# Kernel optimization log

Hardware: AMD Instinct MI355X
Metric: run time of the kernel (lower is better)

## Reference

```python
import jax, jax.numpy as jnp
import numpy as np
from jax import lax

B = 2; H = 96; W = 96
WS = 8; SHIFT = WS // 2; NW = H // WS; P = WS * WS
NH = 3; HD = 32; CD = 96; TD = 96
MID = 2 * CD; GA = 16; BASES = 16

def _rel_index():
    g = np.stack(np.meshgrid(np.arange(WS), np.arange(WS), indexing='ij'), -1).reshape(-1, 2)
    rel = g[:, None, :] - g[None, :, :] + WS - 1
    return jnp.asarray(rel[..., 0] * (2 * WS - 1) + rel[..., 1])  # [P, P]

REL_IDX = _rel_index()

def _sw_mask():
    m = np.zeros((NW, NW, WS, WS, WS, WS), bool); s = WS - SHIFT
    m[-1, :, :s, :, s:, :] = True
    m[-1, :, s:, :, :s, :] = True
    m[:, -1, :, :s, :, s:] = True
    m[:, -1, :, s:, :, :s] = True
    return jnp.asarray(m.reshape(NW * NW, P, P))

SW_MASK = _sw_mask()

def _ln(x, g, b, eps=1e-5):
    mu = x.mean(-1, keepdims=True)
    v = ((x - mu) ** 2).mean(-1, keepdims=True)
    return (x - mu) * lax.rsqrt(v + eps) * g + b

def _conv1x1(x, w):
    return jnp.einsum('bchw,oc->bohw', x, w)

def _conv3x3(x, w, b=None, groups=1):
    y = lax.conv_general_dilated(x, w, (1, 1), ((1, 1), (1, 1)),
                                 dimension_numbers=('NCHW', 'OIHW', 'NCHW'),
                                 feature_group_count=groups)
    return y if b is None else y + b[None, :, None, None]

def _unfold3(x):
    # torch F.unfold(k=3,p=1): channel-major patch order (c, kh, kw)
    bs, c, h, w = x.shape
    xp = jnp.pad(x, ((0, 0), (0, 0), (1, 1), (1, 1)))
    pats = jnp.stack([xp[:, :, i:i + h, j:j + w] for i in range(3) for j in range(3)], axis=2)
    return pats.reshape(bs, c * 9, h * w)

def _adaconv(x, ada_w, p1w, p1b, p2w, p2b):
    bs, c, h, w = x.shape
    para = jax.nn.relu(_conv1x1(x, p1w) + p1b[None, :, None, None])
    para = _conv3x3(para, p2w, p2b).reshape(bs, BASES, h * w)      # [b, r, p]
    xu = _unfold3(x).reshape(bs, GA, (c // GA) * 9, h * w)          # [b, g, d, p]
    # out[b,g,o,p] = sum_{d,r} ada_w[g,o,d,r] * xu[b,g,d,p] * para[b,r,p]
    t = jnp.einsum('godr,bgdp->bgorp', ada_w, xu)
    out = jnp.einsum('bgorp,brp->bgop', t, para)
    return out.reshape(bs, c, h, w)

def _conv_block(x, ln_g, ln_b, c1_pw, c1_dw, c2_pw, ada_w, p1w, p1b, p2w, p2b, c3_w):
    r = _ln(x.transpose(0, 2, 3, 1), ln_g, ln_b).transpose(0, 3, 1, 2)
    b1 = _conv3x3(_conv1x1(r, c1_pw), c1_dw, groups=MID)
    b2 = jax.nn.gelu(_adaconv(_conv1x1(r, c2_pw), ada_w, p1w, p1b, p2w, p2b), approximate=False)
    return x + _conv1x1(b1 * b2, c3_w)

def _wmsa(x, qkv_w, qkv_b, rel_pos, proj_w, proj_b):
    bs = x.shape[0]
    x = jnp.roll(x, (-SHIFT, -SHIFT), (1, 2))
    qkv = jnp.einsum('bhwc,oc->bhwo', x, qkv_w) + qkv_b
    qkv = qkv.reshape(bs, NW, WS, NW, WS, 3, NH, HD)
    qkv = qkv.transpose(5, 6, 0, 1, 3, 2, 4, 7).reshape(3, NH, bs, NW * NW, P, HD)
    q, k, v = qkv[0], qkv[1], qkv[2]
    sim = jnp.einsum('hbwpc,hbwqc->hbwpq', q, k) * (HD ** -0.5)
    bias = rel_pos[REL_IDX.reshape(-1)].reshape(P, P, NH).transpose(2, 0, 1)
    sim = sim + bias[:, None, None]
    sim = jnp.where(SW_MASK[None, None], -jnp.inf, sim)
    attn = jax.nn.softmax(sim, axis=-1)
    out = jnp.einsum('hbwpq,hbwqc->hbwpc', attn, v)
    out = out.reshape(NH, bs, NW, NW, WS, WS, HD).transpose(1, 2, 4, 3, 5, 0, 6).reshape(bs, H, W, NH * HD)
    out = jnp.einsum('bhwc,oc->bhwo', out, proj_w) + proj_b
    return jnp.roll(out, (SHIFT, SHIFT), (1, 2))

def _swin_block(x, ln1_g, ln1_b, qkv_w, qkv_b, rel_pos, proj_w, proj_b,
                ln2_g, ln2_b, f_w1, f_b1, f_dw, f_db, f_w2, f_b2):
    xt = x.transpose(0, 2, 3, 1)  # b h w c
    xt = xt + _wmsa(_ln(xt, ln1_g, ln1_b), qkv_w, qkv_b, rel_pos, proj_w, proj_b)
    y = _ln(xt, ln2_g, ln2_b).transpose(0, 3, 1, 2)
    y = _conv1x1(y, f_w1) + f_b1[None, :, None, None]
    y = _conv3x3(y, f_dw, f_db, groups=2 * TD)
    y = jax.nn.gelu(y, approximate=False)
    y = _conv1x1(y, f_w2) + f_b2[None, :, None, None]
    xt = xt + y.transpose(0, 2, 3, 1)
    return xt.transpose(0, 3, 1, 2)

def _block(x, cb_ln_g, cb_ln_b, cb_c1_pw, cb_c1_dw, cb_c2_pw, ada_w, ada_p1_w, ada_p1_b,
           ada_p2_w, ada_p2_b, cb_c3_w, ln1_g, ln1_b, qkv_w, qkv_b, rel_pos, proj_w, proj_b,
           ln2_g, ln2_b, ffn_w1, ffn_b1, ffn_dw, ffn_db, ffn_w2, ffn_b2, out_w, out_b):
    conv_x, trans_x = x[:, :CD], x[:, CD:]
    conv_x = _conv_block(conv_x, cb_ln_g, cb_ln_b, cb_c1_pw, cb_c1_dw, cb_c2_pw,
                         ada_w, ada_p1_w, ada_p1_b, ada_p2_w, ada_p2_b, cb_c3_w)
    trans_x = _swin_block(trans_x, ln1_g, ln1_b, qkv_w, qkv_b, rel_pos, proj_w, proj_b,
                          ln2_g, ln2_b, ffn_w1, ffn_b1, ffn_dw, ffn_db, ffn_w2, ffn_b2)
    res = _conv1x1(jnp.concatenate([conv_x, trans_x], axis=1), out_w) + out_b[None, :, None, None]
    return x + res

def setup_inputs():
    key = jax.random.key(0)
    ks = jax.random.split(key, 20)
    n = lambda i, shape, s=0.05: jax.random.normal(ks[i], shape, jnp.float32) * s
    return {
        'x': jax.random.normal(ks[0], (B, CD + TD, H, W), jnp.float32),
        'cb_ln_g': jnp.ones((CD,), jnp.float32), 'cb_ln_b': jnp.zeros((CD,), jnp.float32),
        'cb_c1_pw': n(1, (MID, CD)), 'cb_c1_dw': n(2, (MID, 1, 3, 3)),
        'cb_c2_pw': n(3, (MID, CD)),
        'ada_w': n(4, (GA, MID // GA, (MID // GA) * 9, BASES)),
        'ada_p1_w': n(5, (BASES, MID)), 'ada_p1_b': jnp.zeros((BASES,), jnp.float32),
        'ada_p2_w': n(6, (BASES, BASES, 3, 3)), 'ada_p2_b': jnp.zeros((BASES,), jnp.float32),
        'cb_c3_w': n(7, (CD, MID)),
        'ln1_g': jnp.ones((TD,), jnp.float32), 'ln1_b': jnp.zeros((TD,), jnp.float32),
        'qkv_w': n(8, (3 * TD, TD)), 'qkv_b': jnp.zeros((3 * TD,), jnp.float32),
        'rel_pos': n(9, ((2 * WS - 1) ** 2, NH), 0.02),
        'proj_w': n(10, (TD, TD)), 'proj_b': jnp.zeros((TD,), jnp.float32),
        'ln2_g': jnp.ones((TD,), jnp.float32), 'ln2_b': jnp.zeros((TD,), jnp.float32),
        'ffn_w1': n(11, (2 * TD, TD)), 'ffn_b1': jnp.zeros((2 * TD,), jnp.float32),
        'ffn_dw': n(12, (2 * TD, 1, 3, 3)), 'ffn_db': jnp.zeros((2 * TD,), jnp.float32),
        'ffn_w2': n(13, (TD, 2 * TD)), 'ffn_b2': jnp.zeros((TD,), jnp.float32),
        'out_w': n(14, (CD + TD, CD + TD)), 'out_b': jnp.zeros((CD + TD,), jnp.float32),
    }

def reference(x, cb_ln_g, cb_ln_b, cb_c1_pw, cb_c1_dw, cb_c2_pw, ada_w, ada_p1_w, ada_p1_b,
              ada_p2_w, ada_p2_b, cb_c3_w, ln1_g, ln1_b, qkv_w, qkv_b, rel_pos, proj_w, proj_b,
              ln2_g, ln2_b, ffn_w1, ffn_b1, ffn_dw, ffn_db, ffn_w2, ffn_b2, out_w, out_b):
    return _block(x, cb_ln_g, cb_ln_b, cb_c1_pw, cb_c1_dw, cb_c2_pw, ada_w, ada_p1_w, ada_p1_b,
                  ada_p2_w, ada_p2_b, cb_c3_w, ln1_g, ln1_b, qkv_w, qkv_b, rel_pos, proj_w, proj_b,
                  ln2_g, ln2_b, ffn_w1, ffn_b1, ffn_dw, ffn_db, ffn_w2, ffn_b2, out_w, out_b)
```

## Files before the change

kernel.cpp:

```cpp
#include <hip/hip_runtime.h>
#include <math.h>

#define HW_ 9216
#define IH 96
#define IW 96
#define NB 2
#define ST (NB*HW_)

typedef __attribute__((ext_vector_type(8))) short bf16x8;
typedef __attribute__((ext_vector_type(4))) float f32x4;
typedef unsigned short u16;

__device__ __forceinline__ float gelu_f(float v){
  return 0.5f*v*(1.0f+erff(v*0.70710678118654752440f));
}
__device__ __forceinline__ unsigned f2bf(float f){
  unsigned u = __float_as_uint(f);
  return (u + 0x7FFF + ((u>>16)&1)) >> 16;
}
__device__ __forceinline__ float bfl(unsigned u){ return __uint_as_float(u<<16); }
__device__ __forceinline__ float bfh(unsigned u){ return __uint_as_float(u & 0xffff0000u); }

__global__ __launch_bounds__(256) void ln12_k(const float* __restrict__ x,
    const float* __restrict__ g1, const float* __restrict__ b1,
    const float* __restrict__ g2, const float* __restrict__ b2,
    u16* __restrict__ lnc, u16* __restrict__ ln1o,
    float* __restrict__ xc, float* __restrict__ xt)
{
  __shared__ float t[192][33];
  const int p0 = blockIdx.x<<5;
  const int bb = p0/HW_, hw0 = p0 - bb*HW_;
  const int tid = threadIdx.x;
  const int px = tid & 31, cr = tid >> 5;
  const float* xb = x + (size_t)bb*192*HW_ + hw0;
  #pragma unroll
  for (int k=0;k<24;k++){
    int c = cr + k*8;
    t[c][px] = xb[(size_t)c*HW_ + px];
  }
  __syncthreads();
  const int lane = tid&63, wv = tid>>6;
  #pragma unroll 1
  for (int i=0;i<8;i++){
    const int lp = wv*8+i;
    const size_t p = p0 + lp;
    float a0 = t[lane][lp];
    float a1 = (lane<32)? t[64+lane][lp] : 0.f;
    float c0 = t[96+lane][lp];
    float c1 = (lane<32)? t[160+lane][lp] : 0.f;
    float s1=a0+a1, s2=c0+c1;
    #pragma unroll
    for (int o=32;o;o>>=1){ s1+=__shfl_xor(s1,o); s2+=__shfl_xor(s2,o); }
    const float mu1=s1*(1.f/96.f), mu2=s2*(1.f/96.f);
    const float d0=a0-mu1, d1=a1-mu1, e0=c0-mu2, e1=c1-mu2;
    float q1=d0*d0+((lane<32)?d1*d1:0.f), q2=e0*e0+((lane<32)?e1*e1:0.f);
    #pragma unroll
    for (int o=32;o;o>>=1){ q1+=__shfl_xor(q1,o); q2+=__shfl_xor(q2,o); }
    const float r1=rsqrtf(q1*(1.f/96.f)+1e-5f), r2=rsqrtf(q2*(1.f/96.f)+1e-5f);
    lnc [p*96+lane] = (u16)f2bf(d0*r1*g1[lane]+b1[lane]);
    ln1o[p*96+lane] = (u16)f2bf(e0*r2*g2[lane]+b2[lane]);
    xc  [p*96+lane] = a0;
    xt  [p*96+lane] = c0;
    if (lane<32){
      lnc [p*96+64+lane] = (u16)f2bf(d1*r1*g1[64+lane]+b1[64+lane]);
      ln1o[p*96+64+lane] = (u16)f2bf(e1*r2*g2[64+lane]+b2[64+lane]);
      xc  [p*96+64+lane] = a1;
      xt  [p*96+64+lane] = c1;
    }
  }
}

__global__ __launch_bounds__(256) void ln_k(const float* __restrict__ in, int istride,
                                            const float* __restrict__ gam, const float* __restrict__ bet,
                                            u16* __restrict__ out){
  int lane = threadIdx.x & 63;
  int wv   = threadIdx.x >> 6;
  int p    = (blockIdx.x << 2) + wv;
  const float* row = in + (size_t)p*istride;
  float v0 = row[lane];
  float v1 = (lane < 32) ? row[64+lane] : 0.0f;
  float s = v0 + v1;
  #pragma unroll
  for (int o=32;o;o>>=1) s += __shfl_xor(s,o);
  float mu = s * (1.0f/96.0f);
  float d0 = v0 - mu;
  float d1 = v1 - mu;
  float qv = d0*d0 + ((lane<32)? d1*d1 : 0.0f);
  #pragma unroll
  for (int o=32;o;o>>=1) qv += __shfl_xor(qv,o);
  float rstd = rsqrtf(qv*(1.0f/96.0f) + 1e-5f);
  u16* orow = out + (size_t)p*96;
  orow[lane] = (u16)f2bf(d0*rstd*gam[lane] + bet[lane]);
  if (lane < 32) orow[64+lane] = (u16)f2bf(d1*rstd*gam[64+lane] + bet[64+lane]);
}

template<int ACT, bool CONCAT, bool FINAL, bool HASB, bool HASR, bool OUTBF, bool SPLIT>
__global__ __launch_bounds__(256) void conv_mfma_k(
    const u16* __restrict__ in1, const float* __restrict__ in2f, int istride,
    const u16* __restrict__ wbf, const float* __restrict__ bias,
    const float* __restrict__ res, int rstride,
    void* __restrict__ out, int ostride, int Cin, int Cout,
    u16* __restrict__ out2)
{
  __shared__ __align__(16) unsigned char smem[39936];
  unsigned char* actl = smem;
  unsigned char* wl   = smem + 26624;
  const int tid=threadIdx.x, lane=tid&63, wv=tid>>6;
  const int lr=lane&15, g4=lane>>4, wm=wv>>1, wn=wv&1;
  const int p0=blockIdx.x<<7, co0=blockIdx.y<<6;

  f32x4 acc[2][4];
  #pragma unroll
  for (int m=0;m<2;m++)
    #pragma unroll
    for (int n=0;n<4;n++) acc[m][n]=(f32x4){0.f,0.f,0.f,0.f};

  for (int kc=0; kc<Cin; kc+=96){
    {
      const int row=tid>>1, half=tid&1;
      if (!CONCAT || kc==0){
        const u16* rp = in1 + (size_t)(p0+row)*istride + (CONCAT?0:kc) + half*48;
        #pragma unroll
        for (int s=0;s<6;s++)
          *(uint4*)(actl + row*208 + (half*6+s)*16) = *(const uint4*)(rp + s*8);
      } else {
        const float* rp = in2f + (size_t)(p0+row)*96 + half*48;
        #pragma unroll
        for (int s=0;s<6;s++){
          float4 a=*(const float4*)(rp+s*8), b=*(const float4*)(rp+s*8+4);
          uint4 pk;
          pk.x=f2bf(a.x)|(f2bf(a.y)<<16);
          pk.y=f2bf(a.z)|(f2bf(a.w)<<16);
          pk.z=f2bf(b.x)|(f2bf(b.y)<<16);
          pk.w=f2bf(b.z)|(f2bf(b.w)<<16);
          *(uint4*)(actl + row*208 + (half*6+s)*16) = pk;
        }
      }
    }
    {
      const int row=tid&63, grp=tid>>6;
      const int co=co0+row;
      const u16* wr = wbf + (size_t)co*Cin + kc;
      #pragma unroll
      for (int s=0;s<3;s++){
        int sl=grp*3+s;
        uint4 v={0,0,0,0};
        if (co<Cout) v=*(const uint4*)(wr + sl*8);
        *(uint4*)(wl + row*208 + sl*16)=v;
      }
    }
    __syncthreads();
    #pragma unroll
    for (int ks=0;ks<3;ks++){
      const int sl=ks*4+g4;
      bf16x8 afr[2], bfr[4];
      #pragma unroll
      for (int m=0;m<2;m++) afr[m]=*(const bf16x8*)(wl + ((wm*2+m)*16+lr)*208 + sl*16);
      #pragma unroll
      for (int n=0;n<4;n++) bfr[n]=*(const bf16x8*)(actl + (wn*64+n*16+lr)*208 + sl*16);
      #pragma unroll
      for (int m=0;m<2;m++)
        #pragma unroll
        for (int n=0;n<4;n++)
          acc[m][n]=__builtin_amdgcn_mfma_f32_16x16x32_bf16(afr[m], bfr[n], acc[m][n],0,0,0);
    }
    __syncthreads();
  }

  if (FINAL){
    float* outf = (float*)out;
    #pragma unroll
    for (int m=0;m<2;m++){
      const int cb=co0+(wm*2+m)*16+(g4<<2);
      float4 bv = make_float4(0.f,0.f,0.f,0.f);
      if (HASB) bv = *(const float4*)(bias+cb);
      #pragma unroll
      for (int n=0;n<4;n++){
        const int p=p0+wn*64+n*16+lr;
        const int bb=p/HW_, hw=p-bb*HW_;
        const float av[4]={acc[m][n].x,acc[m][n].y,acc[m][n].z,acc[m][n].w};
        const float bvv[4]={bv.x,bv.y,bv.z,bv.w};
        #pragma unroll
        for (int j=0;j<4;j++){
          size_t oi=((size_t)bb*192+cb+j)*HW_+hw;
          outf[oi]=av[j]+bvv[j]+res[oi];
        }
      }
    }
    return;
  }
  float* lt=(float*)smem;
  #pragma unroll
  for (int m=0;m<2;m++)
    #pragma unroll
    for (int n=0;n<4;n++){
      int px=wn*64+n*16+lr;
      int c=(wm*2+m)*16+(g4<<2);
      *(f32x4*)&lt[px*68+c]=acc[m][n];
    }
  __syncthreads();
  {
    const int pr=tid>>1, half=tid&1;
    const int p=p0+pr;
    #pragma unroll
    for (int s=0;s<8;s++){
      int cl=half*32+s*4;
      int co=co0+cl;
      if (co<Cout){
        float4 v=*(float4*)&lt[pr*68+cl];
        if (SPLIT){
          if (co>=384){
            const int c2 = co-384;
            const float4 bv=*(const float4*)(bias+c2);
            v.x=fmaxf(v.x+bv.x,0.f); v.y=fmaxf(v.y+bv.y,0.f);
            v.z=fmaxf(v.z+bv.z,0.f); v.w=fmaxf(v.w+bv.w,0.f);
            uint2 pk;
            pk.x = f2bf(v.x)|(f2bf(v.y)<<16);
            pk.y = f2bf(v.z)|(f2bf(v.w)<<16);
            *(uint2*)((u16*)out + (size_t)p*16 + c2) = pk;
          } else {
            const int cc = (co<192)? co : co-192;
            const int gg = cc/12, cll = cc - gg*12;
            u16* dst = out2 + ((co<192)? (size_t)0 : (size_t)ST*192)
                     + ((size_t)gg*ST + p)*12 + cll;
            uint2 pk;
            pk.x = f2bf(v.x)|(f2bf(v.y)<<16);
            pk.y = f2bf(v.z)|(f2bf(v.w)<<16);
            *(uint2*)dst = pk;
          }
          continue;
        }
        if (HASB){ const float4 bv=*(const float4*)(bias+co); v.x+=bv.x;v.y+=bv.y;v.z+=bv.z;v.w+=bv.w; }
        if (ACT==1){
          v.x=fmaxf(v.x,0.f); v.y=fmaxf(v.y,0.f); v.z=fmaxf(v.z,0.f); v.w=fmaxf(v.w,0.f);
        }
        if (HASR){ const float4 rv=*(const float4*)(res+(size_t)p*rstride+co); v.x+=rv.x;v.y+=rv.y;v.z+=rv.z;v.w+=rv.w; }
        if (OUTBF){
          uint2 pk;
          pk.x = f2bf(v.x)|(f2bf(v.y)<<16);
          pk.y = f2bf(v.z)|(f2bf(v.w)<<16);
          *(uint2*)((u16*)out + (size_t)p*ostride + co) = pk;
        } else {
          *(float4*)((float*)out + (size_t)p*ostride + co) = v;
        }
      }
    }
  }
}

template<bool HASB, bool DOGELU>
__global__ __launch_bounds__(256) void dw3x3_k(const u16* __restrict__ in, int istride,
                                               const float* __restrict__ w,
                                               const float* __restrict__ bias,
                                               u16* __restrict__ out, int C){
  int t = blockIdx.x*256 + threadIdx.x;
  int cg = C >> 2;
  int p = t / cg;
  if (p >= ST) return;
  int c4 = (t - p*cg) << 2;
  int bb = p / HW_, hw = p - bb*HW_;
  int hy = hw / IW, wx = hw - hy*IW;
  float w0[9], w1[9], w2[9], w3[9];
  #pragma unroll
  for (int tp=0;tp<9;tp++){
    w0[tp]=w[(c4+0)*9+tp]; w1[tp]=w[(c4+1)*9+tp]; w2[tp]=w[(c4+2)*9+tp]; w3[tp]=w[(c4+3)*9+tp];
  }
  float ax=0.f, ay=0.f, az=0.f, aw=0.f;
  #pragma unroll
  for (int i=0;i<3;i++){
    int y = hy+i-1;
    if ((unsigned)y >= IH) continue;
    #pragma unroll
    for (int j=0;j<3;j++){
      int x2 = wx+j-1;
      if ((unsigned)x2 >= IW) continue;
      const uint2 r = *(const uint2*)(in + ((size_t)bb*HW_ + y*IW + x2)*istride + c4);
      int tp=i*3+j;
      ax += bfl(r.x)*w0[tp]; ay += bfh(r.x)*w1[tp];
      az += bfl(r.y)*w2[tp]; aw += bfh(r.y)*w3[tp];
    }
  }
  if (HASB){ ax+=bias[c4]; ay+=bias[c4+1]; az+=bias[c4+2]; aw+=bias[c4+3]; }
  if (DOGELU){ ax=gelu_f(ax); ay=gelu_f(ay); az=gelu_f(az); aw=gelu_f(aw); }
  uint2 pk;
  pk.x = f2bf(ax)|(f2bf(ay)<<16);
  pk.y = f2bf(az)|(f2bf(aw)<<16);
  *(uint2*)(out + (size_t)p*C + c4) = pk;
}

__global__ __launch_bounds__(256) void p2conv_k(const u16* __restrict__ in, const float* __restrict__ w,
                                                const float* __restrict__ bias, float* __restrict__ out){
  __shared__ float ws[2304];
  int tid = threadIdx.x;
  for (int i=tid;i<2304;i+=256) ws[i]=w[i];
  __syncthreads();
  int gidx = blockIdx.x*256 + tid;
  int p = gidx >> 2, qq = gidx & 3;
  int bb = p / HW_, hw = p - bb*HW_;
  int hy = hw / IW, wx = hw - hy*IW;
  const int cb = qq<<2;
  float a0=bias[cb], a1=bias[cb+1], a2=bias[cb+2], a3=bias[cb+3];
  #pragma unroll
  for (int i=0;i<3;i++){
    int y=hy+i-1; if ((unsigned)y>=IH) continue;
    #pragma unroll
    for (int j=0;j<3;j++){
      int x2=wx+j-1; if ((unsigned)x2>=IW) continue;
      int tap=i*3+j;
      const uint4 r = *(const uint4*)(in + ((size_t)bb*HW_ + y*IW + x2)*16);
      const uint4 r2 = *(const uint4*)(in + ((size_t)bb*HW_ + y*IW + x2)*16 + 8);
      float vv[16]={bfl(r.x),bfh(r.x),bfl(r.y),bfh(r.y),bfl(r.z),bfh(r.z),bfl(r.w),bfh(r.w),
                    bfl(r2.x),bfh(r2.x),bfl(r2.y),bfh(r2.y),bfl(r2.z),bfh(r2.z),bfl(r2.w),bfh(r2.w)};
      #pragma unroll
      for (int ci=0;ci<16;ci++){
        float v = vv[ci];
        a0 += ws[(cb+0)*144 + ci*9 + tap]*v;
        a1 += ws[(cb+1)*144 + ci*9 + tap]*v;
        a2 += ws[(cb+2)*144 + ci*9 + tap]*v;
        a3 += ws[(cb+3)*144 + ci*9 + tap]*v;
      }
    }
  }
  *(float4*)(out + (size_t)p*16 + cb) = make_float4(a0,a1,a2,a3);
}

__global__ __launch_bounds__(256) void allprep_k(
    const float* __restrict__ s0, const float* __restrict__ s1,
    const float* __restrict__ s2, const float* __restrict__ s3,
    const float* __restrict__ s4, const float* __restrict__ s5,
    const float* __restrict__ s6, const float* __restrict__ s7,
    const float* __restrict__ p1w, const float* __restrict__ aw,
    u16* __restrict__ wdst, u16* __restrict__ apre)
{
  const int bid = blockIdx.x, tid = threadIdx.x;
  if (bid < 648){
    const int blks[8]={108,72,72,72,36,72,72,144};
    const int off[8] ={0,27648,46080,66048,84480,93696,112128,130560};
    const int sz[8]  ={27648,18432,18432,18432,9216,18432,18432,36864};
    int m=0, acc=0;
    #pragma unroll
    for (int k=0;k<8;k++){ if (bid >= acc + blks[k]){ acc += blks[k]; m=k+1; } }
    const float* s = (m==0)?s0:(m==1)?s1:(m==2)?s2:(m==3)?s3:(m==4)?s4:(m==5)?s5:(m==6)?s6:s7;
    int i = (bid-acc)*256 + tid;
    if (i < sz[m]) wdst[off[m]+i] = (u16)f2bf(s[i]);
  } else if (bid < 654){
    int i = (bid-648)*256 + tid;
    if (i < 1536){
      int o = i/96, ci = i - o*96;
      float s = 0.f;
      for (int k=0;k<192;k++) s += p1w[o*192+k]*s2[k*96+ci];
      wdst[64512+i] = (u16)f2bf(s);
    }
  } else {
    int E = (bid-654)*256 + tid;
    int g = E / 30720, e = E - g*30720;
    int row = e / 160, kp = e - row*160;
    int tap = kp >> 4, cl = kp & 15;
    int o = row >> 4, r = row & 15;
    float v = 0.f;
    if (tap < 9 && cl < 12)
      v = aw[(((size_t)(g*12+o)*108) + cl*9 + tap)*16 + r];
    apre[(size_t)g*30720 + e] = (u16)f2bf(v);
  }
}

__global__ __launch_bounds__(256) void adaconv_mfma_k(
    const u16* __restrict__ x1g, const u16* __restrict__ x2g,
    const float* __restrict__ para, const u16* __restrict__ apre,
    const float* __restrict__ dww, u16* __restrict__ outb2)
{
  __shared__ __align__(16) unsigned char smem[34096];
  unsigned char* HB2 = smem;
  unsigned char* HB1 = smem + 8640;
  float* PS = (float*)(smem + 17280);
  float* OS = (float*)(smem + 27520);
  float* WDW = (float*)(smem + 33664);

  const int tid=threadIdx.x, lane=tid&63, wv=tid>>6;
  const int lr=lane&15, g4=lane>>4;
  const int hi=(lane>>5)&1, lo16=(lane>>4)&1;
  const int b=blockIdx.z, g=blockIdx.y, reg=blockIdx.x;
  const int rh=(reg/12)<<4, rw=(reg%12)<<3;

  bf16x8 af[3][5];
  {
    const u16* ag = apre + (size_t)g*30720;
    #pragma unroll
    for (int oo=0;oo<3;oo++){
      const int row=(wv*3+oo)*16+lr;
      #pragma unroll
      for (int ks=0;ks<5;ks++)
        af[oo][ks] = *(const bf16x8*)(ag + row*160 + ks*32 + g4*8);
    }
  }
  if (tid < 180){
    int hy = tid/10, hx = tid - hy*10;
    int gy = rh+hy-1, gx = rw+hx-1;
    uint2 a2={0,0},b2={0,0},c2={0,0}, a1={0,0},b1={0,0},c1={0,0};
    if ((unsigned)gy<IH && (unsigned)gx<IW){
      const size_t base = ((size_t)g*ST + (size_t)b*HW_ + gy*IW + gx)*12;
      const u16* s2 = x2g + base;
      a2=*(const uint2*)s2; b2=*(const uint2*)(s2+4); c2=*(const uint2*)(s2+8);
      const u16* s1 = x1g + base;
      a1=*(const uint2*)s1; b1=*(const uint2*)(s1+4); c1=*(const uint2*)(s1+8);
    }
    *(uint4*)(HB2 + tid*48)      = make_uint4(a2.x,a2.y,b2.x,b2.y);
    *(uint4*)(HB2 + tid*48 + 16) = make_uint4(c2.x,c2.y,0,0);
    *(uint4*)(HB1 + tid*48)      = make_uint4(a1.x,a1.y,b1.x,b1.y);
    *(uint4*)(HB1 + tid*48 + 16) = make_uint4(c1.x,c1.y,0,0);
  }
  if (tid < 108) WDW[tid] = dww[g*108 + tid];
  #pragma unroll
  for (int it=0; it<2; ++it){
    int idx = tid + (it<<8);
    int sub = idx >> 8;
    int p = (idx>>2)&63, q = idx&3;
    int gy = rh + (sub<<3) + (p>>3), gx = rw + (p&7);
    float4 v = *(const float4*)(para + ((size_t)b*HW_+gy*IW+gx)*16 + q*4);
    *(float4*)&PS[sub*1280 + p*20 + q*4] = v;
  }
  __syncthreads();

  int tapoff[5];
  tapoff[0] = hi ? 48   : 0;
  tapoff[1] = hi ? 480  : 96;
  tapoff[2] = hi ? 576  : 528;
  tapoff[3] = hi ? 1008 : 960;
  tapoff[4] = 1056;

  #pragma unroll
  for (int sub=0; sub<2; ++sub){
    const int sy = sub<<3;
    const int base0 = ((sy + (lr>>3))*10 + (lr&7))*48 + lo16*16;

    f32x4 acc[3][4];
    #pragma unroll
    for (int oo=0;oo<3;oo++)
      #pragma unroll
      for (int n=0;n<4;n++) acc[oo][n]=(f32x4){0.f,0.f,0.f,0.f};

    #pragma unroll
    for (int ks=0;ks<5;ks++){
      bf16x8 bfr[4];
      #pragma unroll
      for (int n=0;n<4;n++)
        bfr[n] = *(const bf16x8*)(HB2 + base0 + n*960 + tapoff[ks]);
      #pragma unroll
      for (int oo=0;oo<3;oo++)
        #pragma unroll
        for (int n=0;n<4;n++)
          acc[oo][n]=__builtin_amdgcn_mfma_f32_16x16x32_bf16(af[oo][ks], bfr[n], acc[oo][n],0,0,0);
    }

    const float* ps = &PS[sub*1280];
    #pragma unroll
    for (int oo=0;oo<3;oo++){
      const int o=wv*3+oo;
      #pragma unroll
      for (int n=0;n<4;n++){
        const int p=(n<<4)+lr;
        const f32x4 prv = *(const f32x4*)&ps[p*20+(g4<<2)];
        float s=acc[oo][n].x*prv.x+acc[oo][n].y*prv.y+acc[oo][n].z*prv.z+acc[oo][n].w*prv.w;
        s += __shfl_xor(s,16); s += __shfl_xor(s,32);
        if (g4==n) OS[((sub<<6)+p)*12+o] = gelu_f(s);
      }
    }
  }
  __syncthreads();
  {
    const size_t gb = (size_t)b*HW_;
    for (int idx=tid; idx<384; idx+=256){
      const int cq = idx % 3;
      const int rest = idx / 3;
      const int p = rest & 63, sub = rest >> 6;
      const int py = p>>3, px = p&7;
      const int Y = (sub<<3)+py, X = px;
      const unsigned char* hb1 = HB1 + (Y*10+X)*48 + cq*8;
      const float* wd = &WDW[cq*36];
      float v0=0.f,v1=0.f,v2=0.f,v3=0.f;
      #pragma unroll
      for (int i=0;i<3;i++){
        #pragma unroll
        for (int j=0;j<3;j++){
          const uint2 r = *(const uint2*)(hb1 + (i*10+j)*48);
          const int tp=i*3+j;
          v0 += bfl(r.x)*wd[tp];      v1 += bfh(r.x)*wd[9+tp];
          v2 += bfl(r.y)*wd[18+tp];   v3 += bfh(r.y)*wd[27+tp];
        }
      }
      const size_t gi = (gb + (rh+(sub<<3)+py)*IW + (rw+px))*192 + g*12 + cq*4;
      const float* os = &OS[((sub<<6)+p)*12 + cq*4];
      uint2 pk;
      pk.x = f2bf(os[0]*v0) | (f2bf(os[1]*v1)<<16);
      pk.y = f2bf(os[2]*v2) | (f2bf(os[3]*v3)<<16);
      *(uint2*)(outb2 + gi) = pk;
    }
  }
}

__global__ __launch_bounds__(64) void attn_k(const u16* __restrict__ qkv,
                                             const float* __restrict__ relpos,
                                             u16* __restrict__ outa){
  __shared__ float k_s[2048];
  __shared__ float v_s[2048];
  __shared__ float rel_s[225];
  const int win = blockIdx.x, head = blockIdx.y, b = blockIdx.z;
  const int wi = win/12, wj = win%12;
  const int lane = threadIdx.x;
  for (int i=lane;i<225;i+=64) rel_s[i] = relpos[i*3+head];
  const int pi = lane>>3, pj = lane&7;
  const int hr = wi*8+pi, wr = wj*8+pj;
  const int sh = (hr+4)%96, sw = (wr+4)%96;
  const size_t pix = (size_t)b*HW_ + sh*96 + sw;
  const u16* base = qkv + pix*288;
  const float SC = 0.17677669529663687f;
  float q[32];
  #pragma unroll
  for (int i=0;i<4;i++){
    const uint4 r = *(const uint4*)(base + head*32 + i*8);
    q[i*8+0]=bfl(r.x)*SC; q[i*8+1]=bfh(r.x)*SC;
    q[i*8+2]=bfl(r.y)*SC; q[i*8+3]=bfh(r.y)*SC;
    q[i*8+4]=bfl(r.z)*SC; q[i*8+5]=bfh(r.z)*SC;
    q[i*8+6]=bfl(r.w)*SC; q[i*8+7]=bfh(r.w)*SC;
  }
  #pragma unroll
  for (int i=0;i<4;i++){
    const uint4 rk = *(const uint4*)(base + 96 + head*32 + i*8);
    const uint4 rv = *(const uint4*)(base + 192 + head*32 + i*8);
    *(float4*)&k_s[(lane<<5)+i*8]   = make_float4(bfl(rk.x),bfh(rk.x),bfl(rk.y),bfh(rk.y));
    *(float4*)&k_s[(lane<<5)+i*8+4] = make_float4(bfl(rk.z),bfh(rk.z),bfl(rk.w),bfh(rk.w));
    *(float4*)&v_s[(lane<<5)+i*8]   = make_float4(bfl(rv.x),bfh(rv.x),bfl(rv.y),bfh(rv.y));
    *(float4*)&v_s[(lane<<5)+i*8+4] = make_float4(bfl(rv.z),bfh(rv.z),bfl(rv.w),bfh(rv.w));
  }
  __syncthreads();
  const bool mi = (wi==11), mj = (wj==11);
  float sc[64];
  #pragma unroll
  for (int qq=0; qq<64; qq++){
    const float4* kr4 = (const float4*)&k_s[qq<<5];
    float s = 0.f;
    #pragma unroll
    for (int i=0;i<8;i++){
      const float4 kv = kr4[i];
      s += q[4*i]*kv.x + q[4*i+1]*kv.y + q[4*i+2]*kv.z + q[4*i+3]*kv.w;
    }
    const int qi = qq>>3, qj = qq&7;
    s += rel_s[(pi-qi+7)*15 + (pj-qj+7)];
    const bool msk = (mi && ((pi<4)!=(qi<4))) || (mj && ((pj<4)!=(qj<4)));
    sc[qq] = msk ? -1e30f : s;
  }
  float m = sc[0];
  #pragma unroll
  for (int qq=1;qq<64;qq++) m = fmaxf(m, sc[qq]);
  float sum = 0.f;
  #pragma unroll
  for (int qq=0;qq<64;qq++){ float e = __expf(sc[qq]-m); sc[qq]=e; sum+=e; }
  const float inv = 1.f/sum;
  float acc[32];
  #pragma unroll
  for (int i=0;i<32;i++) acc[i]=0.f;
  #pragma unroll
  for (int qq=0;qq<64;qq++){
    const float a = sc[qq]*inv;
    const float4* vr4 = (const float4*)&v_s[qq<<5];
    #pragma unroll
    for (int i=0;i<8;i++){
      const float4 vv = vr4[i];
      acc[4*i]+=a*vv.x; acc[4*i+1]+=a*vv.y; acc[4*i+2]+=a*vv.z; acc[4*i+3]+=a*vv.w;
    }
  }
  u16* orow = outa + pix*96 + head*32;
  #pragma unroll
  for (int i=0;i<4;i++){
    uint4 pk;
    pk.x = f2bf(acc[i*8+0])|(f2bf(acc[i*8+1])<<16);
    pk.y = f2bf(acc[i*8+2])|(f2bf(acc[i*8+3])<<16);
    pk.z = f2bf(acc[i*8+4])|(f2bf(acc[i*8+5])<<16);
    pk.w = f2bf(acc[i*8+6])|(f2bf(acc[i*8+7])<<16);
    *(uint4*)(orow + i*8) = pk;
  }
}

extern "C" void kernel_launch(void* const* d_in, const int* in_sizes, int n_in,
                              void* d_out, int out_size, void* d_ws, size_t ws_size,
                              hipStream_t stream)
{
  (void)in_sizes; (void)n_in; (void)out_size; (void)ws_size;
  const float* x        = (const float*)d_in[0];
  const float* cb_ln_g  = (const float*)d_in[1];
  const float* cb_ln_b  = (const float*)d_in[2];
  const float* cb_c1_pw = (const float*)d_in[3];
  const float* cb_c1_dw = (const float*)d_in[4];
  const float* cb_c2_pw = (const float*)d_in[5];
  const float* ada_w    = (const float*)d_in[6];
  const float* ada_p1_w = (const float*)d_in[7];
  const float* ada_p1_b = (const float*)d_in[8];
  const float* ada_p2_w = (const float*)d_in[9];
  const float* ada_p2_b = (const float*)d_in[10];
  const float* cb_c3_w  = (const float*)d_in[11];
  const float* ln1_g    = (const float*)d_in[12];
  const float* ln1_b    = (const float*)d_in[13];
  const float* qkv_w    = (const float*)d_in[14];
  const float* qkv_b    = (const float*)d_in[15];
  const float* rel_pos  = (const float*)d_in[16];
  const float* proj_w   = (const float*)d_in[17];
  const float* proj_b   = (const float*)d_in[18];
  const float* ln2_g    = (const float*)d_in[19];
  const float* ln2_b    = (const float*)d_in[20];
  const float* ffn_w1   = (const float*)d_in[21];
  const float* ffn_b1   = (const float*)d_in[22];
  const float* ffn_dw   = (const float*)d_in[23];
  const float* ffn_db   = (const float*)d_in[24];
  const float* ffn_w2   = (const float*)d_in[25];
  const float* ffn_b2   = (const float*)d_in[26];
  const float* out_w    = (const float*)d_in[27];
  const float* out_b    = (const float*)d_in[28];

  char* wsb = (char*)d_ws;
  float* XC  = (float*)wsb;
  float* U0f = (float*)(wsb + (size_t)ST*96*4);
  float* XT  = (float*)(wsb + (size_t)ST*384*4);
  float* PA2 = (float*)(wsb + (size_t)ST*480*4);
  u16* B2b  = (u16*)(wsb + (size_t)ST*496*4);
  u16* LNCb = B2b  + (size_t)ST*192;
  u16* R4b  = LNCb + (size_t)ST*96;
  u16* R6b  = R4b  + (size_t)ST*96;
  u16* PA1b = R6b  + (size_t)ST*96;
  u16* Wbf  = PA1b + (size_t)ST*16;
  u16* Apre = Wbf + 167424;
  u16* X1G  = (u16*)U0f;
  u16* X2G  = X1G + (size_t)ST*192;
  u16* QKVb = (u16*)U0f;
  u16* FF1b = (u16*)U0f;
  u16* DWOb = (u16*)U0f + (size_t)ST*192;

  const u16* W_qkv  = Wbf + 0;
  const u16* W_c12p = Wbf + 27648;
  const u16* W_c3   = Wbf + 66048;
  const u16* W_proj = Wbf + 84480;
  const u16* W_ffn1 = Wbf + 93696;
  const u16* W_ffn2 = Wbf + 112128;
  const u16* W_fin  = Wbf + 130560;

  allprep_k<<<2574, 256, 0, stream>>>(qkv_w, cb_c1_pw, cb_c2_pw, cb_c3_w,
                                      proj_w, ffn_w1, ffn_w2, out_w,
                                      ada_p1_w, ada_w, Wbf, Apre);

  ln12_k<<<ST/32, 256, 0, stream>>>(x, cb_ln_g, cb_ln_b, ln1_g, ln1_b, LNCb, R6b, XC, XT);

  conv_mfma_k<0,false,false,false,false,true,true><<<dim3(ST/128, 7), 256, 0, stream>>>(LNCb, nullptr, 96, W_c12p, ada_p1_b, nullptr, 0, PA1b, 16, 96, 400, X1G);
  p2conv_k<<<(ST*4)/256, 256, 0, stream>>>(PA1b, ada_p2_w, ada_p2_b, PA2);
  adaconv_mfma_k<<<dim3(72, 16, NB), 256, 0, stream>>>(X1G, X2G, PA2, Apre, cb_c1_dw, B2b);
  conv_mfma_k<0,false,false,false,true,true,false><<<dim3(ST/128, 2), 256, 0, stream>>>(B2b, nullptr, 192, W_c3, nullptr, XC, 96, R4b, 96, 192, 96, nullptr);

  conv_mfma_k<0,false,false,true,false,true,false><<<dim3(ST/128, 5), 256, 0, stream>>>(R6b, nullptr, 96, W_qkv, qkv_b, nullptr, 0, QKVb, 288, 96, 288, nullptr);
  attn_k<<<dim3(144, 3, NB), 64, 0, stream>>>(QKVb, rel_pos, R6b);
  conv_mfma_k<0,false,false,true,true,false,false><<<dim3(ST/128, 2), 256, 0, stream>>>(R6b, nullptr, 96, W_proj, proj_b, XT, 96, XT, 96, 96, 96, nullptr);
  ln_k<<<ST/4, 256, 0, stream>>>(XT, 96, ln2_g, ln2_b, R6b);
  conv_mfma_k<0,false,false,true,false,true,false><<<dim3(ST/128, 3), 256, 0, stream>>>(R6b, nullptr, 96, W_ffn1, ffn_b1, nullptr, 0, FF1b, 192, 96, 192, nullptr);
  dw3x3_k<true,true><<<(ST*48)/256, 256, 0, stream>>>(FF1b, 192, ffn_dw, ffn_db, DWOb, 192);
  conv_mfma_k<0,false,false,true,true,false,false><<<dim3(ST/128, 2), 256, 0, stream>>>(DWOb, nullptr, 192, W_ffn2, ffn_b2, XT, 96, XT, 96, 192, 96, nullptr);

  conv_mfma_k<0,true,true,true,true,false,false><<<dim3(ST/128, 3), 256, 0, stream>>>(R4b, XT, 96, W_fin, out_b, x, 0, (float*)d_out, 0, 192, 192, nullptr);
}
```

Measured before the change: 230.1 us.

## Merge independent kernels into combined launches to cut launch count

Kernel bodies become device functions, and independent stages share one launch through block-index dispatch. Weight prep runs with the first LayerNorm, the adaconv-p1 GEMM with the QKV GEMM, adaconv with the attention projection, and conv3 with the second LayerNorm. Attention moves earlier, and QKV gets its own workspace region because it is now live at the same time as X1G. The aim is to remove launch gaps and let small grids fill the GPU together. The cost is a larger workspace footprint and mixed block types within one launch, which may share resources unevenly.

```diff
diff --git a/kernel.cpp b/kernel.cpp
--- a/kernel.cpp
+++ b/kernel.cpp
@@ -21,14 +21,14 @@
 __device__ __forceinline__ float bfl(unsigned u){ return __uint_as_float(u<<16); }
 __device__ __forceinline__ float bfh(unsigned u){ return __uint_as_float(u & 0xffff0000u); }
 
-__global__ __launch_bounds__(256) void ln12_k(const float* __restrict__ x,
+__device__ __forceinline__ void ln12_body(const float* __restrict__ x,
     const float* __restrict__ g1, const float* __restrict__ b1,
     const float* __restrict__ g2, const float* __restrict__ b2,
     u16* __restrict__ lnc, u16* __restrict__ ln1o,
-    float* __restrict__ xc, float* __restrict__ xt)
+    float* __restrict__ xc, float* __restrict__ xt, int bidx)
 {
   __shared__ float t[192][33];
-  const int p0 = blockIdx.x<<5;
+  const int p0 = bidx<<5;
   const int bb = p0/HW_, hw0 = p0 - bb*HW_;
   const int tid = threadIdx.x;
   const int px = tid & 31, cr = tid >> 5;
@@ -70,12 +70,13 @@
   }
 }
 
-__global__ __launch_bounds__(256) void ln_k(const float* __restrict__ in, int istride,
-                                            const float* __restrict__ gam, const float* __restrict__ bet,
-                                            u16* __restrict__ out){
+__device__ __forceinline__ void ln_body(const float* __restrict__ in, int istride,
+    const float* __restrict__ gam, const float* __restrict__ bet,
+    u16* __restrict__ out, int bidx)
+{
   int lane = threadIdx.x & 63;
   int wv   = threadIdx.x >> 6;
-  int p    = (blockIdx.x << 2) + wv;
+  int p    = (bidx << 2) + wv;
   const float* row = in + (size_t)p*istride;
   float v0 = row[lane];
   float v1 = (lane < 32) ? row[64+lane] : 0.0f;
@@ -95,19 +96,18 @@
 }
 
 template<int ACT, bool CONCAT, bool FINAL, bool HASB, bool HASR, bool OUTBF, bool SPLIT>
-__global__ __launch_bounds__(256) void conv_mfma_k(
+__device__ __forceinline__ void conv_body(unsigned char* smem,
     const u16* __restrict__ in1, const float* __restrict__ in2f, int istride,
     const u16* __restrict__ wbf, const float* __restrict__ bias,
     const float* __restrict__ res, int rstride,
     void* __restrict__ out, int ostride, int Cin, int Cout,
-    u16* __restrict__ out2)
-{
-  __shared__ __align__(16) unsigned char smem[39936];
+    u16* __restrict__ out2, int bx, int by)
+{
   unsigned char* actl = smem;
   unsigned char* wl   = smem + 26624;
   const int tid=threadIdx.x, lane=tid&63, wv=tid>>6;
   const int lr=lane&15, g4=lane>>4, wm=wv>>1, wn=wv&1;
-  const int p0=blockIdx.x<<7, co0=blockIdx.y<<6;
+  const int p0=bx<<7, co0=by<<6;
 
   f32x4 acc[2][4];
   #pragma unroll
@@ -248,128 +248,25 @@
   }
 }
 
-template<bool HASB, bool DOGELU>
-__global__ __launch_bounds__(256) void dw3x3_k(const u16* __restrict__ in, int istride,
-                                               const float* __restrict__ w,
-                                               const float* __restrict__ bias,
-                                               u16* __restrict__ out, int C){
-  int t = blockIdx.x*256 + threadIdx.x;
-  int cg = C >> 2;
-  int p = t / cg;
-  if (p >= ST) return;
-  int c4 = (t - p*cg) << 2;
-  int bb = p / HW_, hw = p - bb*HW_;
-  int hy = hw / IW, wx = hw - hy*IW;
-  float w0[9], w1[9], w2[9], w3[9];
-  #pragma unroll
-  for (int tp=0;tp<9;tp++){
-    w0[tp]=w[(c4+0)*9+tp]; w1[tp]=w[(c4+1)*9+tp]; w2[tp]=w[(c4+2)*9+tp]; w3[tp]=w[(c4+3)*9+tp];
-  }
-  float ax=0.f, ay=0.f, az=0.f, aw=0.f;
-  #pragma unroll
-  for (int i=0;i<3;i++){
-    int y = hy+i-1;
-    if ((unsigned)y >= IH) continue;
-    #pragma unroll
-    for (int j=0;j<3;j++){
-      int x2 = wx+j-1;
-      if ((unsigned)x2 >= IW) continue;
-      const uint2 r = *(const uint2*)(in + ((size_t)bb*HW_ + y*IW + x2)*istride + c4);
-      int tp=i*3+j;
-      ax += bfl(r.x)*w0[tp]; ay += bfh(r.x)*w1[tp];
-      az += bfl(r.y)*w2[tp]; aw += bfh(r.y)*w3[tp];
-    }
-  }
-  if (HASB){ ax+=bias[c4]; ay+=bias[c4+1]; az+=bias[c4+2]; aw+=bias[c4+3]; }
-  if (DOGELU){ ax=gelu_f(ax); ay=gelu_f(ay); az=gelu_f(az); aw=gelu_f(aw); }
-  uint2 pk;
-  pk.x = f2bf(ax)|(f2bf(ay)<<16);
-  pk.y = f2bf(az)|(f2bf(aw)<<16);
-  *(uint2*)(out + (size_t)p*C + c4) = pk;
-}
-
-__global__ __launch_bounds__(256) void p2conv_k(const u16* __restrict__ in, const float* __restrict__ w,
-                                                const float* __restrict__ bias, float* __restrict__ out){
-  __shared__ float ws[2304];
-  int tid = threadIdx.x;
-  for (int i=tid;i<2304;i+=256) ws[i]=w[i];
-  __syncthreads();
-  int gidx = blockIdx.x*256 + tid;
-  int p = gidx >> 2, qq = gidx & 3;
-  int bb = p / HW_, hw = p - bb*HW_;
-  int hy = hw / IW, wx = hw - hy*IW;
-  const int cb = qq<<2;
-  float a0=bias[cb], a1=bias[cb+1], a2=bias[cb+2], a3=bias[cb+3];
-  #pragma unroll
-  for (int i=0;i<3;i++){
-    int y=hy+i-1; if ((unsigned)y>=IH) continue;
-    #pragma unroll
-    for (int j=0;j<3;j++){
-      int x2=wx+j-1; if ((unsigned)x2>=IW) continue;
-      int tap=i*3+j;
-      const uint4 r = *(const uint4*)(in + ((size_t)bb*HW_ + y*IW + x2)*16);
-      const uint4 r2 = *(const uint4*)(in + ((size_t)bb*HW_ + y*IW + x2)*16 + 8);
-      float vv[16]={bfl(r.x),bfh(r.x),bfl(r.y),bfh(r.y),bfl(r.z),bfh(r.z),bfl(r.w),bfh(r.w),
-                    bfl(r2.x),bfh(r2.x),bfl(r2.y),bfh(r2.y),bfl(r2.z),bfh(r2.z),bfl(r2.w),bfh(r2.w)};
-      #pragma unroll
-      for (int ci=0;ci<16;ci++){
-        float v = vv[ci];
-        a0 += ws[(cb+0)*144 + ci*9 + tap]*v;
-        a1 += ws[(cb+1)*144 + ci*9 + tap]*v;
-        a2 += ws[(cb+2)*144 + ci*9 + tap]*v;
-        a3 += ws[(cb+3)*144 + ci*9 + tap]*v;
-      }
-    }
-  }
-  *(float4*)(out + (size_t)p*16 + cb) = make_float4(a0,a1,a2,a3);
-}
-
-__global__ __launch_bounds__(256) void allprep_k(
-    const float* __restrict__ s0, const float* __restrict__ s1,
-    const float* __restrict__ s2, const float* __restrict__ s3,
-    const float* __restrict__ s4, const float* __restrict__ s5,
-    const float* __restrict__ s6, const float* __restrict__ s7,
-    const float* __restrict__ p1w, const float* __restrict__ aw,
-    u16* __restrict__ wdst, u16* __restrict__ apre)
-{
-  const int bid = blockIdx.x, tid = threadIdx.x;
-  if (bid < 648){
-    const int blks[8]={108,72,72,72,36,72,72,144};
-    const int off[8] ={0,27648,46080,66048,84480,93696,112128,130560};
-    const int sz[8]  ={27648,18432,18432,18432,9216,18432,18432,36864};
-    int m=0, acc=0;
-    #pragma unroll
-    for (int k=0;k<8;k++){ if (bid >= acc + blks[k]){ acc += blks[k]; m=k+1; } }
-    const float* s = (m==0)?s0:(m==1)?s1:(m==2)?s2:(m==3)?s3:(m==4)?s4:(m==5)?s5:(m==6)?s6:s7;
-    int i = (bid-acc)*256 + tid;
-    if (i < sz[m]) wdst[off[m]+i] = (u16)f2bf(s[i]);
-  } else if (bid < 654){
-    int i = (bid-648)*256 + tid;
-    if (i < 1536){
-      int o = i/96, ci = i - o*96;
-      float s = 0.f;
-      for (int k=0;k<192;k++) s += p1w[o*192+k]*s2[k*96+ci];
-      wdst[64512+i] = (u16)f2bf(s);
-    }
-  } else {
-    int E = (bid-654)*256 + tid;
-    int g = E / 30720, e = E - g*30720;
-    int row = e / 160, kp = e - row*160;
-    int tap = kp >> 4, cl = kp & 15;
-    int o = row >> 4, r = row & 15;
-    float v = 0.f;
-    if (tap < 9 && cl < 12)
-      v = aw[(((size_t)(g*12+o)*108) + cl*9 + tap)*16 + r];
-    apre[(size_t)g*30720 + e] = (u16)f2bf(v);
-  }
-}
-
-__global__ __launch_bounds__(256) void adaconv_mfma_k(
+template<int ACT, bool CONCAT, bool FINAL, bool HASB, bool HASR, bool OUTBF, bool SPLIT>
+__global__ __launch_bounds__(256) void conv_mfma_k(
+    const u16* __restrict__ in1, const float* __restrict__ in2f, int istride,
+    const u16* __restrict__ wbf, const float* __restrict__ bias,
+    const float* __restrict__ res, int rstride,
+    void* __restrict__ out, int ostride, int Cin, int Cout,
+    u16* __restrict__ out2)
+{
+  __shared__ __align__(16) unsigned char smem[39936];
+  conv_body<ACT,CONCAT,FINAL,HASB,HASR,OUTBF,SPLIT>(smem, in1, in2f, istride, wbf, bias,
+      res, rstride, out, ostride, Cin, Cout, out2, blockIdx.x, blockIdx.y);
+}
+
+__device__ __forceinline__ void adaconv_body(unsigned char* smem,
     const u16* __restrict__ x1g, const u16* __restrict__ x2g,
     const float* __restrict__ para, const u16* __restrict__ apre,
-    const float* __restrict__ dww, u16* __restrict__ outb2)
-{
-  __shared__ __align__(16) unsigned char smem[34096];
+    const float* __restrict__ dww, u16* __restrict__ outb2,
+    int b, int g, int reg)
+{
   unsigned char* HB2 = smem;
   unsigned char* HB1 = smem + 8640;
   float* PS = (float*)(smem + 17280);
@@ -379,7 +276,6 @@
   const int tid=threadIdx.x, lane=tid&63, wv=tid>>6;
   const int lr=lane&15, g4=lane>>4;
   const int hi=(lane>>5)&1, lo16=(lane>>4)&1;
-  const int b=blockIdx.z, g=blockIdx.y, reg=blockIdx.x;
   const int rh=(reg/12)<<4, rw=(reg%12)<<3;
 
   bf16x8 af[3][5];
@@ -496,6 +392,181 @@
       *(uint2*)(outb2 + gi) = pk;
     }
   }
+}
+
+__device__ __forceinline__ void allprep_body(
+    const float* __restrict__ s0, const float* __restrict__ s1,
+    const float* __restrict__ s2, const float* __restrict__ s3,
+    const float* __restrict__ s4, const float* __restrict__ s5,
+    const float* __restrict__ s6, const float* __restrict__ s7,
+    const float* __restrict__ p1w, const float* __restrict__ aw,
+    u16* __restrict__ wdst, u16* __restrict__ apre, int bid)
+{
+  const int tid = threadIdx.x;
+  if (bid < 648){
+    const int blks[8]={108,72,72,72,36,72,72,144};
+    const int off[8] ={0,27648,46080,66048,84480,93696,112128,130560};
+    const int sz[8]  ={27648,18432,18432,18432,9216,18432,18432,36864};
+    int m=0, acc=0;
+    #pragma unroll
+    for (int k=0;k<8;k++){ if (bid >= acc + blks[k]){ acc += blks[k]; m=k+1; } }
+    const float* s = (m==0)?s0:(m==1)?s1:(m==2)?s2:(m==3)?s3:(m==4)?s4:(m==5)?s5:(m==6)?s6:s7;
+    int i = (bid-acc)*256 + tid;
+    if (i < sz[m]) wdst[off[m]+i] = (u16)f2bf(s[i]);
+  } else if (bid < 654){
+    int i = (bid-648)*256 + tid;
+    if (i < 1536){
+      int o = i/96, ci = i - o*96;
+      float s = 0.f;
+      for (int k=0;k<192;k++) s += p1w[o*192+k]*s2[k*96+ci];
+      wdst[64512+i] = (u16)f2bf(s);
+    }
+  } else {
+    int E = (bid-654)*256 + tid;
+    int g = E / 30720, e = E - g*30720;
+    int row = e / 160, kp = e - row*160;
+    int tap = kp >> 4, cl = kp & 15;
+    int o = row >> 4, r = row & 15;
+    float v = 0.f;
+    if (tap < 9 && cl < 12)
+      v = aw[(((size_t)(g*12+o)*108) + cl*9 + tap)*16 + r];
+    apre[(size_t)g*30720 + e] = (u16)f2bf(v);
+  }
+}
+
+__global__ __launch_bounds__(256) void prep_ln12_k(
+    const float* s0, const float* s1, const float* s2, const float* s3,
+    const float* s4, const float* s5, const float* s6, const float* s7,
+    const float* p1w, const float* aw, u16* wdst, u16* apre,
+    const float* x, const float* g1, const float* b1,
+    const float* g2, const float* b2,
+    u16* lnc, u16* ln1o, float* xc, float* xt)
+{
+  const int bid = blockIdx.x;
+  if (bid < 2574)
+    allprep_body(s0,s1,s2,s3,s4,s5,s6,s7,p1w,aw,wdst,apre,bid);
+  else
+    ln12_body(x,g1,b1,g2,b2,lnc,ln1o,xc,xt,bid-2574);
+}
+
+__global__ __launch_bounds__(256) void gemm12_k(
+    const u16* lnc, const u16* r6, const u16* wc12p, const float* p1b,
+    const u16* wqkv, const float* qkvb, u16* pa1, u16* x1g, u16* qkv)
+{
+  __shared__ __align__(16) unsigned char smem[39936];
+  if (blockIdx.y < 7)
+    conv_body<0,false,false,false,false,true,true>(smem, lnc, nullptr, 96, wc12p, p1b,
+        nullptr, 0, pa1, 16, 96, 400, x1g, blockIdx.x, blockIdx.y);
+  else
+    conv_body<0,false,false,true,false,true,false>(smem, r6, nullptr, 96, wqkv, qkvb,
+        nullptr, 0, qkv, 288, 96, 288, nullptr, blockIdx.x, blockIdx.y-7);
+}
+
+__global__ __launch_bounds__(256) void ada_proj_k(
+    const u16* x1g, const u16* x2g, const float* para, const u16* apre,
+    const float* dww, u16* outb2,
+    const u16* r6, const u16* wproj, const float* projb, float* xt)
+{
+  __shared__ __align__(16) unsigned char smem[39936];
+  const int bid = blockIdx.x;
+  if (bid < 2304){
+    const int b = bid / 1152, rem = bid - b*1152;
+    const int g = rem / 72, reg = rem - g*72;
+    adaconv_body(smem, x1g, x2g, para, apre, dww, outb2, b, g, reg);
+  } else {
+    const int bx = bid - 2304;
+    conv_body<0,false,false,true,true,false,false>(smem, r6, nullptr, 96, wproj, projb,
+        xt, 96, xt, 96, 96, 96, nullptr, bx % 144, bx / 144);
+  }
+}
+
+__global__ __launch_bounds__(256) void c3_ln2_k(
+    const u16* b2b, const u16* wc3, const float* xc, u16* r4,
+    const float* xt, const float* g2, const float* bt2, u16* r6)
+{
+  __shared__ __align__(16) unsigned char smem[39936];
+  const int bid = blockIdx.x;
+  if (bid < 288)
+    conv_body<0,false,false,false,true,true,false>(smem, b2b, nullptr, 192, wc3, nullptr,
+        xc, 96, r4, 96, 192, 96, nullptr, bid % 144, bid / 144);
+  else
+    ln_body(xt, 96, g2, bt2, r6, bid-288);
+}
+
+template<bool HASB, bool DOGELU>
+__global__ __launch_bounds__(256) void dw3x3_k(const u16* __restrict__ in, int istride,
+                                               const float* __restrict__ w,
+                                               const float* __restrict__ bias,
+                                               u16* __restrict__ out, int C){
+  int t = blockIdx.x*256 + threadIdx.x;
+  int cg = C >> 2;
+  int p = t / cg;
+  if (p >= ST) return;
+  int c4 = (t - p*cg) << 2;
+  int bb = p / HW_, hw = p - bb*HW_;
+  int hy = hw / IW, wx = hw - hy*IW;
+  float w0[9], w1[9], w2[9], w3[9];
+  #pragma unroll
+  for (int tp=0;tp<9;tp++){
+    w0[tp]=w[(c4+0)*9+tp]; w1[tp]=w[(c4+1)*9+tp]; w2[tp]=w[(c4+2)*9+tp]; w3[tp]=w[(c4+3)*9+tp];
+  }
+  float ax=0.f, ay=0.f, az=0.f, aw=0.f;
+  #pragma unroll
+  for (int i=0;i<3;i++){
+    int y = hy+i-1;
+    if ((unsigned)y >= IH) continue;
+    #pragma unroll
+    for (int j=0;j<3;j++){
+      int x2 = wx+j-1;
+      if ((unsigned)x2 >= IW) continue;
+      const uint2 r = *(const uint2*)(in + ((size_t)bb*HW_ + y*IW + x2)*istride + c4);
+      int tp=i*3+j;
+      ax += bfl(r.x)*w0[tp]; ay += bfh(r.x)*w1[tp];
+      az += bfl(r.y)*w2[tp]; aw += bfh(r.y)*w3[tp];
+    }
+  }
+  if (HASB){ ax+=bias[c4]; ay+=bias[c4+1]; az+=bias[c4+2]; aw+=bias[c4+3]; }
+  if (DOGELU){ ax=gelu_f(ax); ay=gelu_f(ay); az=gelu_f(az); aw=gelu_f(aw); }
+  uint2 pk;
+  pk.x = f2bf(ax)|(f2bf(ay)<<16);
+  pk.y = f2bf(az)|(f2bf(aw)<<16);
+  *(uint2*)(out + (size_t)p*C + c4) = pk;
+}
+
+__global__ __launch_bounds__(256) void p2conv_k(const u16* __restrict__ in, const float* __restrict__ w,
+                                                const float* __restrict__ bias, float* __restrict__ out){
+  __shared__ float ws[2304];
+  int tid = threadIdx.x;
+  for (int i=tid;i<2304;i+=256) ws[i]=w[i];
+  __syncthreads();
+  int gidx = blockIdx.x*256 + tid;
+  int p = gidx >> 2, qq = gidx & 3;
+  int bb = p / HW_, hw = p - bb*HW_;
+  int hy = hw / IW, wx = hw - hy*IW;
+  const int cb = qq<<2;
+  float a0=bias[cb], a1=bias[cb+1], a2=bias[cb+2], a3=bias[cb+3];
+  #pragma unroll
+  for (int i=0;i<3;i++){
+    int y=hy+i-1; if ((unsigned)y>=IH) continue;
+    #pragma unroll
+    for (int j=0;j<3;j++){
+      int x2=wx+j-1; if ((unsigned)x2>=IW) continue;
+      int tap=i*3+j;
+      const uint4 r = *(const uint4*)(in + ((size_t)bb*HW_ + y*IW + x2)*16);
+      const uint4 r2 = *(const uint4*)(in + ((size_t)bb*HW_ + y*IW + x2)*16 + 8);
+      float vv[16]={bfl(r.x),bfh(r.x),bfl(r.y),bfh(r.y),bfl(r.z),bfh(r.z),bfl(r.w),bfh(r.w),
+                    bfl(r2.x),bfh(r2.x),bfl(r2.y),bfh(r2.y),bfl(r2.z),bfh(r2.z),bfl(r2.w),bfh(r2.w)};
+      #pragma unroll
+      for (int ci=0;ci<16;ci++){
+        float v = vv[ci];
+        a0 += ws[(cb+0)*144 + ci*9 + tap]*v;
+        a1 += ws[(cb+1)*144 + ci*9 + tap]*v;
+        a2 += ws[(cb+2)*144 + ci*9 + tap]*v;
+        a3 += ws[(cb+3)*144 + ci*9 + tap]*v;
+      }
+    }
+  }
+  *(float4*)(out + (size_t)p*16 + cb) = make_float4(a0,a1,a2,a3);
 }
 
 __global__ __launch_bounds__(64) void attn_k(const u16* __restrict__ qkv,
@@ -628,9 +699,9 @@
   u16* PA1b = R6b  + (size_t)ST*96;
   u16* Wbf  = PA1b + (size_t)ST*16;
   u16* Apre = Wbf + 167424;
+  u16* QKVb = Apre + 491520;
   u16* X1G  = (u16*)U0f;
   u16* X2G  = X1G + (size_t)ST*192;
-  u16* QKVb = (u16*)U0f;
   u16* FF1b = (u16*)U0f;
   u16* DWOb = (u16*)U0f + (size_t)ST*192;
 
@@ -642,24 +713,26 @@
   const u16* W_ffn2 = Wbf + 112128;
   const u16* W_fin  = Wbf + 130560;
 
-  allprep_k<<<2574, 256, 0, stream>>>(qkv_w, cb_c1_pw, cb_c2_pw, cb_c3_w,
-                                      proj_w, ffn_w1, ffn_w2, out_w,
-                                      ada_p1_w, ada_w, Wbf, Apre);
-
-  ln12_k<<<ST/32, 256, 0, stream>>>(x, cb_ln_g, cb_ln_b, ln1_g, ln1_b, LNCb, R6b, XC, XT);
-
-  conv_mfma_k<0,false,false,false,false,true,true><<<dim3(ST/128, 7), 256, 0, stream>>>(LNCb, nullptr, 96, W_c12p, ada_p1_b, nullptr, 0, PA1b, 16, 96, 400, X1G);
+  prep_ln12_k<<<3150, 256, 0, stream>>>(qkv_w, cb_c1_pw, cb_c2_pw, cb_c3_w,
+                                        proj_w, ffn_w1, ffn_w2, out_w,
+                                        ada_p1_w, ada_w, Wbf, Apre,
+                                        x, cb_ln_g, cb_ln_b, ln1_g, ln1_b,
+                                        LNCb, R6b, XC, XT);
+
+  gemm12_k<<<dim3(144, 12), 256, 0, stream>>>(LNCb, R6b, W_c12p, ada_p1_b,
+                                              W_qkv, qkv_b, PA1b, X1G, QKVb);
+
+  attn_k<<<dim3(144, 3, NB), 64, 0, stream>>>(QKVb, rel_pos, R6b);
   p2conv_k<<<(ST*4)/256, 256, 0, stream>>>(PA1b, ada_p2_w, ada_p2_b, PA2);
-  adaconv_mfma_k<<<dim3(72, 16, NB), 256, 0, stream>>>(X1G, X2G, PA2, Apre, cb_c1_dw, B2b);
-  conv_mfma_k<0,false,false,false,true,true,false><<<dim3(ST/128, 2), 256, 0, stream>>>(B2b, nullptr, 192, W_c3, nullptr, XC, 96, R4b, 96, 192, 96, nullptr);
-
-  conv_mfma_k<0,false,false,true,false,true,false><<<dim3(ST/128, 5), 256, 0, stream>>>(R6b, nullptr, 96, W_qkv, qkv_b, nullptr, 0, QKVb, 288, 96, 288, nullptr);
-  attn_k<<<dim3(144, 3, NB), 64, 0, stream>>>(QKVb, rel_pos, R6b);
-  conv_mfma_k<0,false,false,true,true,false,false><<<dim3(ST/128, 2), 256, 0, stream>>>(R6b, nullptr, 96, W_proj, proj_b, XT, 96, XT, 96, 96, 96, nullptr);
-  ln_k<<<ST/4, 256, 0, stream>>>(XT, 96, ln2_g, ln2_b, R6b);
-  conv_mfma_k<0,false,false,true,false,true,false><<<dim3(ST/128, 3), 256, 0, stream>>>(R6b, nullptr, 96, W_ffn1, ffn_b1, nullptr, 0, FF1b, 192, 96, 192, nullptr);
+
+  ada_proj_k<<<2592, 256, 0, stream>>>(X1G, X2G, PA2, Apre, cb_c1_dw, B2b,
+                                       R6b, W_proj, proj_b, XT);
+
+  c3_ln2_k<<<4896, 256, 0, stream>>>(B2b, W_c3, XC, R4b, XT, ln2_g, ln2_b, R6b);
+
+  conv_mfma_k<0,false,false,true,false,true,false><<<dim3(144, 3), 256, 0, stream>>>(R6b, nullptr, 96, W_ffn1, ffn_b1, nullptr, 0, FF1b, 192, 96, 192, nullptr);
   dw3x3_k<true,true><<<(ST*48)/256, 256, 0, stream>>>(FF1b, 192, ffn_dw, ffn_db, DWOb, 192);
-  conv_mfma_k<0,false,false,true,true,false,false><<<dim3(ST/128, 2), 256, 0, stream>>>(DWOb, nullptr, 192, W_ffn2, ffn_b2, XT, 96, XT, 96, 192, 96, nullptr);
-
-  conv_mfma_k<0,true,true,true,true,false,false><<<dim3(ST/128, 3), 256, 0, stream>>>(R4b, XT, 96, W_fin, out_b, x, 0, (float*)d_out, 0, 192, 192, nullptr);
-}
+  conv_mfma_k<0,false,false,true,true,false,false><<<dim3(144, 2), 256, 0, stream>>>(DWOb, nullptr, 192, W_ffn2, ffn_b2, XT, 96, XT, 96, 192, 96, nullptr);
+
+  conv_mfma_k<0,true,true,true,true,false,false><<<dim3(144, 3), 256, 0, stream>>>(R4b, XT, 96, W_fin, out_b, x, 0, (float*)d_out, 0, 192, 192, nullptr);
+}
```

Result: faster. 207.0 us (-10.0%).
